# Performance work log

Hardware: AMD Instinct MI355X
Metric: run time of the kernel (lower is better)

The kernel has to match this reference:

```python
import jax, jax.numpy as jnp
import numpy as np

B, D_IN, D_H, D_OUT, D_INT = 1024, 2048, 4096, 2048, 1024


def fwht(x):
    """Fast Walsh-Hadamard transform over a length-2^k vector (unnormalized),
    faithful to the torch chunk/cat butterfly loop."""
    n = x.shape[0]
    k = int(n).bit_length() - 1
    for i in range(k):
        y = x.reshape(2 ** i, 2, -1)        # split butterfly level i
        x = jnp.stack([y[:, 0] + y[:, 1], y[:, 0] - y[:, 1]], axis=1)
    return x.reshape(n)


def fastfood(V, BB, Pi, GG, DD):
    """fastfood_torched: pad -> B*x -> H -> permute -> G* -> H -> slice/scale."""
    LL = BB.shape[0]
    vpad = jnp.zeros((LL,), V.dtype).at[: V.shape[0]].set(V)
    m5 = fwht(fwht(BB * vpad)[Pi] * GG)
    divisor = jnp.sqrt(LL * jnp.sum(GG * GG))
    return m5[:DD] / (divisor * np.sqrt(float(DD) / LL))


def _ff_vars(key, DD):
    LL = 1 << int(np.ceil(np.log2(DD)))
    k1, k2, k3 = jax.random.split(key, 3)
    BB = jnp.where(jax.random.uniform(k1, (LL,)) < 0.5, -1.0, 1.0).astype(jnp.float32)
    Pi = jax.random.permutation(k2, LL).astype(jnp.int32)
    GG = jax.random.normal(k3, (LL,), dtype=jnp.float32)
    return BB, Pi, GG


def setup_inputs():
    key = jax.random.key(0)
    ks = jax.random.split(key, 8)
    x = jax.random.normal(ks[0], (B, D_IN), dtype=jnp.float32)
    V = jax.random.normal(ks[1], (D_INT,), dtype=jnp.float32) * 0.01
    W1_0 = jax.random.normal(ks[2], (D_H, D_IN), dtype=jnp.float32) * 0.02
    b1_0 = jnp.zeros((D_H,), jnp.float32)
    W2_0 = jax.random.normal(ks[3], (D_OUT, D_H), dtype=jnp.float32) * 0.02
    b2_0 = jnp.zeros((D_OUT,), jnp.float32)
    BB_W1, Pi_W1, GG_W1 = _ff_vars(ks[4], D_H * D_IN)
    BB_b1, Pi_b1, GG_b1 = _ff_vars(ks[5], D_H)
    BB_W2, Pi_W2, GG_W2 = _ff_vars(ks[6], D_OUT * D_H)
    BB_b2, Pi_b2, GG_b2 = _ff_vars(ks[7], D_OUT)
    return dict(x=x, V=V, W1_0=W1_0, b1_0=b1_0, W2_0=W2_0, b2_0=b2_0,
                BB_W1=BB_W1, Pi_W1=Pi_W1, GG_W1=GG_W1,
                BB_b1=BB_b1, Pi_b1=Pi_b1, GG_b1=GG_b1,
                BB_W2=BB_W2, Pi_W2=Pi_W2, GG_W2=GG_W2,
                BB_b2=BB_b2, Pi_b2=Pi_b2, GG_b2=GG_b2)


def reference(x, V, W1_0, b1_0, W2_0, b2_0,
              BB_W1, Pi_W1, GG_W1, BB_b1, Pi_b1, GG_b1,
              BB_W2, Pi_W2, GG_W2, BB_b2, Pi_b2, GG_b2):
    # Reconstruct each parameter: theta = theta0 + fastfood(V).view(shape)
    W1 = W1_0 + fastfood(V, BB_W1, Pi_W1, GG_W1, D_H * D_IN).reshape(D_H, D_IN)
    b1 = b1_0 + fastfood(V, BB_b1, Pi_b1, GG_b1, D_H)
    W2 = W2_0 + fastfood(V, BB_W2, Pi_W2, GG_W2, D_OUT * D_H).reshape(D_OUT, D_H)
    b2 = b2_0 + fastfood(V, BB_b2, Pi_b2, GG_b2, D_OUT)
    # Wrapped module forward (2-layer MLP)
    h = jax.nn.relu(x @ W1.T + b1)
    return h @ W2.T + b2
```

## Files before the change

kernel.cpp:

```cpp
#include <hip/hip_runtime.h>
#include <hip/hip_bf16.h>
#include <stdint.h>


typedef __attribute__((ext_vector_type(8))) short bf16x8;
typedef __attribute__((ext_vector_type(4))) float f32x4;

__device__ __forceinline__ ushort f2bf(float f) {
  union { float f; uint32_t u; } v; v.f = f;
  return (ushort)((v.u + 0x7FFFu + ((v.u >> 16) & 1u)) >> 16);
}
__device__ __forceinline__ float bf2f(ushort u) {
  union { uint32_t u; float f; } v; v.u = (uint32_t)u << 16; return v.f;
}

__device__ __forceinline__ void gload_lds16(const void* g, void* l) {
  __builtin_amdgcn_global_load_lds(
      (const __attribute__((address_space(1))) void*)g,
      (__attribute__((address_space(3))) void*)l, 16, 0, 0);
}

template <int NN>
__device__ __forceinline__ void wht_inreg(float* v) {
#pragma unroll
  for (int h = 1; h < NN; h <<= 1)
#pragma unroll
    for (int g = 0; g < NN; g += (h << 1))
#pragma unroll
      for (int k = 0; k < h; ++k) {
        float a = v[g + k], b = v[g + k + h];
        v[g + k] = a + b; v[g + k + h] = a - b;
      }
}

__global__ __launch_bounds__(256) void make_t_kernel(
    const float* __restrict__ V, const float* __restrict__ BB1,
    const float* __restrict__ BB2, float* __restrict__ t1, float* __restrict__ t2) {
  __shared__ float ts[1024];
  const float* BB = blockIdx.x ? BB2 : BB1;
  float* t = blockIdx.x ? t2 : t1;
  int tid = threadIdx.x;
  for (int i = tid; i < 1024; i += 256) ts[i] = BB[i] * V[i];
  for (int st = 0; st < 10; ++st) {
    int half = 1 << st;
    __syncthreads();
    for (int j = tid; j < 512; j += 256) {
      int p = ((j >> st) << (st + 1)) | (j & (half - 1));
      float a = ts[p], b = ts[p + half];
      ts[p] = a + b; ts[p + half] = a - b;
    }
  }
  __syncthreads();
  for (int i = tid; i < 1024; i += 256) t[i] = ts[i];
}

__global__ __launch_bounds__(256) void make_bias_kernel(
    const float* __restrict__ V,
    const float* __restrict__ BB1, const int* __restrict__ Pi1, const float* __restrict__ GG1, const float* __restrict__ b10,
    const float* __restrict__ BB2, const int* __restrict__ Pi2, const float* __restrict__ GG2, const float* __restrict__ b20,
    float* __restrict__ ob1, float* __restrict__ ob2) {
  __shared__ float ts[1024];
  __shared__ float zs[4096];
  __shared__ float red[4];
  int tid = threadIdx.x;
  int which = blockIdx.x;
  int L = which ? 2048 : 4096;
  const float* BB = which ? BB2 : BB1;
  const int* Pi = which ? Pi2 : Pi1;
  const float* GG = which ? GG2 : GG1;
  const float* b0 = which ? b20 : b10;
  float* ob = which ? ob2 : ob1;

  for (int i = tid; i < 1024; i += 256) ts[i] = BB[i] * V[i];
  for (int st = 0; st < 10; ++st) {
    int half = 1 << st;
    __syncthreads();
    for (int j = tid; j < 512; j += 256) {
      int p = ((j >> st) << (st + 1)) | (j & (half - 1));
      float a = ts[p], b = ts[p + half];
      ts[p] = a + b; ts[p + half] = a - b;
    }
  }
  __syncthreads();
  float gsum = 0.f;
  for (int i = tid; i < L; i += 256) {
    int pi = Pi[i];
    float g = GG[i];
    gsum += g * g;
    zs[i] = ts[pi & 1023] * g;
  }
  for (int o = 32; o > 0; o >>= 1) gsum += __shfl_down(gsum, o);
  if ((tid & 63) == 0) red[tid >> 6] = gsum;
  __syncthreads();
  float ssum = red[0] + red[1] + red[2] + red[3];
  for (int st = 0; (1 << st) < L; ++st) {
    int half = 1 << st;
    __syncthreads();
    for (int j = tid; j < (L >> 1); j += 256) {
      int p = ((j >> st) << (st + 1)) | (j & (half - 1));
      float a = zs[p], b = zs[p + half];
      zs[p] = a + b; zs[p + half] = a - b;
    }
  }
  __syncthreads();
  float scale = rsqrtf((float)L * ssum);
  for (int i = tid; i < L; i += 256) ob[i] = b0[i] + zs[i] * scale;
}

__global__ __launch_bounds__(256) void ff_pass1(
    const int* __restrict__ Pi, const float* __restrict__ GG,
    const float* __restrict__ t, ushort* __restrict__ inter, float* __restrict__ partials) {
  __shared__ float ts[1024];
  __shared__ float zs[8448];
  __shared__ float red[4];
  int tid = threadIdx.x;
  size_t base = (size_t)blockIdx.x * 8192;
  for (int i = tid; i < 1024; i += 256) ts[i] = t[i];
  __syncthreads();
  float gsum = 0.f;
#pragma unroll 8
  for (int ii = 0; ii < 32; ++ii) {
    int i = ii * 256 + tid;
    int pi = Pi[base + i];
    float g = GG[base + i];
    gsum += g * g;
    zs[i + (i >> 5)] = ts[pi & 1023] * g;
  }
  for (int o = 32; o > 0; o >>= 1) gsum += __shfl_down(gsum, o);
  if ((tid & 63) == 0) red[tid >> 6] = gsum;
  __syncthreads();
  if (tid == 0) partials[blockIdx.x] = red[0] + red[1] + red[2] + red[3];

  float v[32];
  {
    int b0 = tid << 5;
#pragma unroll
    for (int r = 0; r < 32; ++r) { int i = b0 + r; v[r] = zs[i + (i >> 5)]; }
    wht_inreg<32>(v);
#pragma unroll
    for (int r = 0; r < 32; ++r) { int i = b0 + r; zs[i + (i >> 5)] = v[r]; }
  }
  __syncthreads();
  {
    int lo = tid & 31, hi = tid >> 5;
#pragma unroll
    for (int r = 0; r < 32; ++r) { int i = lo | (r << 5) | (hi << 10); v[r] = zs[i + (i >> 5)]; }
    wht_inreg<32>(v);
#pragma unroll
    for (int r = 0; r < 32; ++r) { int i = lo | (r << 5) | (hi << 10); zs[i + (i >> 5)] = v[r]; }
  }
  __syncthreads();
  {
    float w[32];
#pragma unroll
    for (int q = 0; q < 4; ++q)
#pragma unroll
      for (int r = 0; r < 8; ++r) { int i = tid + (q << 8) + (r << 10); w[q * 8 + r] = zs[i + (i >> 5)]; }
#pragma unroll
    for (int q = 0; q < 4; ++q) wht_inreg<8>(w + 8 * q);
#pragma unroll
    for (int q = 0; q < 4; ++q)
#pragma unroll
      for (int r = 0; r < 8; ++r)
        inter[base + tid + (q << 8) + (r << 10)] = f2bf(w[q * 8 + r]);
  }
}

__global__ __launch_bounds__(1024) void ff_pass2(
    const ushort* __restrict__ inter, const float* __restrict__ W0,
    const float* __restrict__ partials, ushort* __restrict__ Wb) {
  __shared__ float tile[1024 * 33];
  __shared__ float red2[16];
  int tid = threadIdx.x;
  int cb = blockIdx.x * 32;
  float s = partials[tid];
  for (int o = 32; o > 0; o >>= 1) s += __shfl_down(s, o);
  if ((tid & 63) == 0) red2[tid >> 6] = s;
#pragma unroll
  for (int it = 0; it < 8; ++it) {
    int u = it * 1024 + tid;
    int row = u >> 3, c4 = u & 7;
    ushort4 d = *(const ushort4*)(inter + (size_t)row * 8192 + cb + (c4 << 2));
    float* tp = &tile[row * 33 + (c4 << 2)];
    tp[0] = bf2f(d.x); tp[1] = bf2f(d.y); tp[2] = bf2f(d.z); tp[3] = bf2f(d.w);
  }
  __syncthreads();
  float ssum = 0.f;
#pragma unroll
  for (int k = 0; k < 16; ++k) ssum += red2[k];
  float sc = rsqrtf(8388608.f * ssum);

  float v[32];
  int c = tid & 31, g = tid >> 5;
#pragma unroll
  for (int r = 0; r < 32; ++r) v[r] = tile[(32 * g + r) * 33 + c];
  wht_inreg<32>(v);
#pragma unroll
  for (int r = 0; r < 32; ++r) tile[(32 * g + r) * 33 + c] = v[r];
  __syncthreads();
#pragma unroll
  for (int r = 0; r < 32; ++r) v[r] = tile[((r << 5) + g) * 33 + c];
  wht_inreg<32>(v);
#pragma unroll
  for (int r = 0; r < 32; ++r) {
    size_t gg = (size_t)((r << 5) + g) * 8192 + cb + c;
    Wb[gg] = f2bf(v[r] * sc + W0[gg]);
  }
}

__global__ __launch_bounds__(256) void cvt_f32_bf16(
    const float4* __restrict__ in, ushort4* __restrict__ out, int n4) {
  int i = blockIdx.x * 256 + threadIdx.x;
  if (i < n4) {
    float4 v = in[i];
    ushort4 o;
    o.x = f2bf(v.x); o.y = f2bf(v.y); o.z = f2bf(v.z); o.w = f2bf(v.w);
    out[i] = o;
  }
}

template <int EPI>
__global__ __launch_bounds__(256) void gemm_bt(
    const ushort* __restrict__ A, const ushort* __restrict__ B,
    const float* __restrict__ bias, ushort* __restrict__ Cb, float* __restrict__ Cf,
    int M, int N, int K, int nt) {
  __shared__ ushort As[2][128 * 64];
  __shared__ ushort Bs[2][128 * 64];
  const int tid = threadIdx.x;
  const int w = tid >> 6, l = tid & 63;
  const int wr = w >> 1, wc = w & 1;
  const int brow = blockIdx.y << 7, bcol = blockIdx.x << 7;
  const int lrow = l >> 3;
  const int csrc = ((l & 7) ^ lrow) << 3;
  const int l15 = l & 15;
  const int x7 = l15 & 7;
  const int kb = blockIdx.z * (nt << 6);
  f32x4 acc[4][4] = {};

  const ushort* pa = A + (size_t)(brow + (w << 5) + lrow) * K + kb + csrc;
  const ushort* pb = B + (size_t)(bcol + (w << 5) + lrow) * K + kb + csrc;
  const size_t K8 = (size_t)K << 3;

#define STAGE(buf, tt)                                                      \
  {                                                                         \
    const ushort* qa = pa + ((tt) << 6);                                    \
    const ushort* qb = pb + ((tt) << 6);                                    \
    _Pragma("unroll")                                                       \
    for (int i = 0; i < 4; ++i) {                                           \
      gload_lds16(qa + K8 * i, &As[buf][(((w << 2) + i) << 9)]);            \
      gload_lds16(qb + K8 * i, &Bs[buf][(((w << 2) + i) << 9)]);            \
    }                                                                       \
  }

  STAGE(0, 0);
  __syncthreads();
  for (int t = 0; t < nt; ++t) {
    int cur = t & 1;
    if (t + 1 < nt) STAGE(cur ^ 1, t + 1);
#pragma unroll
    for (int kk = 0; kk < 2; ++kk) {
      bf16x8 af[4], bfr[4];
      int c8 = (kk << 2) + (l >> 4);
#pragma unroll
      for (int m = 0; m < 4; ++m) {
        int ra = (wr << 6) + (m << 4) + l15;
        af[m] = *(const bf16x8*)&As[cur][(ra << 6) + ((c8 ^ x7) << 3)];
      }
#pragma unroll
      for (int n = 0; n < 4; ++n) {
        int rb = (wc << 6) + (n << 4) + l15;
        bfr[n] = *(const bf16x8*)&Bs[cur][(rb << 6) + ((c8 ^ x7) << 3)];
      }
#pragma unroll
      for (int m = 0; m < 4; ++m)
#pragma unroll
        for (int n = 0; n < 4; ++n)
          acc[m][n] = __builtin_amdgcn_mfma_f32_16x16x32_bf16(af[m], bfr[n], acc[m][n], 0, 0, 0);
    }
    __syncthreads();
  }
#undef STAGE

  if (EPI == 0) {
#pragma unroll
    for (int n = 0; n < 4; ++n) {
      int col = bcol + (wc << 6) + (n << 4) + l15;
      float bv = bias[col];
#pragma unroll
      for (int m = 0; m < 4; ++m) {
        int row0 = brow + (wr << 6) + (m << 4) + ((l >> 4) << 2);
#pragma unroll
        for (int j = 0; j < 4; ++j) {
          float vv = fmaxf(acc[m][n][j] + bv, 0.f);
          Cb[(size_t)(row0 + j) * N + col] = f2bf(vv);
        }
      }
    }
  } else {
    float* outp = Cf + (size_t)blockIdx.z * M * N;
#pragma unroll
    for (int n = 0; n < 4; ++n) {
      int col = bcol + (wc << 6) + (n << 4) + l15;
#pragma unroll
      for (int m = 0; m < 4; ++m) {
        int row0 = brow + (wr << 6) + (m << 4) + ((l >> 4) << 2);
#pragma unroll
        for (int j = 0; j < 4; ++j)
          outp[(size_t)(row0 + j) * N + col] = acc[m][n][j];
      }
    }
  }
}

__global__ __launch_bounds__(256) void reduce_out(
    const float4* __restrict__ P, const float* __restrict__ b2,
    float4* __restrict__ out) {
  int i = blockIdx.x * 256 + threadIdx.x;
  float4 a = P[i], b = P[i + 524288];
  const float4 bb = *(const float4*)(b2 + ((i & 511) << 2));
  float4 o;
  o.x = a.x + b.x + bb.x; o.y = a.y + b.y + bb.y;
  o.z = a.z + b.z + bb.z; o.w = a.w + b.w + bb.w;
  out[i] = o;
}

extern "C" void kernel_launch(void* const* d_in, const int* in_sizes, int n_in,
                              void* d_out, int out_size, void* d_ws, size_t ws_size,
                              hipStream_t stream) {
  const float* x     = (const float*)d_in[0];
  const float* V     = (const float*)d_in[1];
  const float* W1_0  = (const float*)d_in[2];
  const float* b1_0  = (const float*)d_in[3];
  const float* W2_0  = (const float*)d_in[4];
  const float* b2_0  = (const float*)d_in[5];
  const float* BB_W1 = (const float*)d_in[6];
  const int*   Pi_W1 = (const int*)d_in[7];
  const float* GG_W1 = (const float*)d_in[8];
  const float* BB_b1 = (const float*)d_in[9];
  const int*   Pi_b1 = (const int*)d_in[10];
  const float* GG_b1 = (const float*)d_in[11];
  const float* BB_W2 = (const float*)d_in[12];
  const int*   Pi_W2 = (const int*)d_in[13];
  const float* GG_W2 = (const float*)d_in[14];
  const float* BB_b2 = (const float*)d_in[15];
  const int*   Pi_b2 = (const int*)d_in[16];
  const float* GG_b2 = (const float*)d_in[17];
  float* out = (float*)d_out;

  const size_t MB = 1048576ull;
  char* ws = (char*)d_ws;
  ushort* inter = (ushort*)(ws);
  float*  P     = (float*)(ws);
  ushort* W1b   = (ushort*)(ws + 16 * MB);
  ushort* W2b   = (ushort*)(ws + 32 * MB);
  ushort* xb    = (ushort*)(ws + 48 * MB);
  ushort* hb    = (ushort*)(ws + 52 * MB);
  char*   S     = ws + 60 * MB;
  float*  t1    = (float*)(S);
  float*  t2    = (float*)(S + 4096);
  float*  b1    = (float*)(S + 8192);
  float*  b2    = (float*)(S + 8192 + 16384);
  float*  parts = (float*)(S + 8192 + 16384 + 8192);

  make_t_kernel<<<2, 256, 0, stream>>>(V, BB_W1, BB_W2, t1, t2);
  make_bias_kernel<<<2, 256, 0, stream>>>(V, BB_b1, Pi_b1, GG_b1, b1_0,
                                          BB_b2, Pi_b2, GG_b2, b2_0, b1, b2);
  cvt_f32_bf16<<<2048, 256, 0, stream>>>((const float4*)x, (ushort4*)xb, 524288);

  ff_pass1<<<1024, 256, 0, stream>>>(Pi_W1, GG_W1, t1, inter, parts);
  ff_pass2<<<256, 1024, 0, stream>>>(inter, W1_0, parts, W1b);
  ff_pass1<<<1024, 256, 0, stream>>>(Pi_W2, GG_W2, t2, inter, parts);
  ff_pass2<<<256, 1024, 0, stream>>>(inter, W2_0, parts, W2b);

  gemm_bt<0><<<dim3(32, 8, 1), 256, 0, stream>>>(xb, W1b, b1, hb, nullptr, 1024, 4096, 2048, 32);
  gemm_bt<1><<<dim3(16, 8, 2), 256, 0, stream>>>(hb, W2b, nullptr, nullptr, P, 1024, 2048, 4096, 32);
  reduce_out<<<2048, 256, 0, stream>>>((const float4*)P, b2, (float4*)out);
}
```

Before: 184.8 us.

## Batch fastfood passes for both weights, vectorize accesses, deepen GEMM pipeline

The W1 and W2 fastfood passes now run as single launches with twice the blocks, replacing two pairs of launches. Global loads and stores in both passes are widened to 16-byte vectors, and the WHT stage index mapping in pass1 is changed so the bf16 output can be stored contiguously. Pass2 now stages its result through LDS before writing coalesced short8 stores. The GEMM goes from a 2-stage to a 4-stage LDS ring with hand-placed vmcnt waits and raw barriers, which makes LDS use larger and depends on correct waitcnt accounting.

```diff
diff --git a/kernel.cpp b/kernel.cpp
--- a/kernel.cpp
+++ b/kernel.cpp
@@ -4,6 +4,7 @@
 
 
 typedef __attribute__((ext_vector_type(8))) short bf16x8;
+typedef __attribute__((ext_vector_type(8))) short short8;
 typedef __attribute__((ext_vector_type(4))) float f32x4;
 
 __device__ __forceinline__ ushort f2bf(float f) {
@@ -19,6 +20,12 @@
       (const __attribute__((address_space(1))) void*)g,
       (__attribute__((address_space(3))) void*)l, 16, 0, 0);
 }
+
+__device__ __forceinline__ void wait_vm16() { asm volatile("s_waitcnt vmcnt(16)" ::: "memory"); }
+__device__ __forceinline__ void wait_vm8()  { asm volatile("s_waitcnt vmcnt(8)"  ::: "memory"); }
+__device__ __forceinline__ void wait_vm0()  { asm volatile("s_waitcnt vmcnt(0)"  ::: "memory"); }
+__device__ __forceinline__ void wait_lgkm0(){ asm volatile("s_waitcnt lgkmcnt(0)" ::: "memory"); }
+__device__ __forceinline__ void barrier_raw(){ asm volatile("s_barrier" ::: "memory"); }
 
 template <int NN>
 __device__ __forceinline__ void wht_inreg(float* v) {
@@ -108,23 +115,42 @@
 }
 
 __global__ __launch_bounds__(256) void ff_pass1(
-    const int* __restrict__ Pi, const float* __restrict__ GG,
-    const float* __restrict__ t, ushort* __restrict__ inter, float* __restrict__ partials) {
+    const int* __restrict__ Pi1, const float* __restrict__ GG1,
+    const int* __restrict__ Pi2, const float* __restrict__ GG2,
+    const float* __restrict__ t1, const float* __restrict__ t2,
+    ushort* __restrict__ inter1, ushort* __restrict__ inter2,
+    float* __restrict__ partials) {
   __shared__ float ts[1024];
   __shared__ float zs[8448];
   __shared__ float red[4];
   int tid = threadIdx.x;
-  size_t base = (size_t)blockIdx.x * 8192;
+  int wsel = blockIdx.x >> 10;
+  int blk = blockIdx.x & 1023;
+  const int* Pi = wsel ? Pi2 : Pi1;
+  const float* GG = wsel ? GG2 : GG1;
+  const float* t = wsel ? t2 : t1;
+  ushort* inter = wsel ? inter2 : inter1;
+  size_t base = (size_t)blk * 8192;
+
   for (int i = tid; i < 1024; i += 256) ts[i] = t[i];
   __syncthreads();
+
+  const int4* Pi4 = (const int4*)(Pi + base);
+  const float4* GG4 = (const float4*)(GG + base);
   float gsum = 0.f;
-#pragma unroll 8
-  for (int ii = 0; ii < 32; ++ii) {
-    int i = ii * 256 + tid;
-    int pi = Pi[base + i];
-    float g = GG[base + i];
-    gsum += g * g;
-    zs[i + (i >> 5)] = ts[pi & 1023] * g;
+#pragma unroll
+  for (int q = 0; q < 8; ++q) {
+    int u = (q << 8) + tid;
+    int4 p4 = Pi4[u];
+    float4 g4 = GG4[u];
+    gsum += g4.x * g4.x + g4.y * g4.y + g4.z * g4.z + g4.w * g4.w;
+    int i0 = u << 2;
+    float4 z;
+    z.x = ts[p4.x & 1023] * g4.x;
+    z.y = ts[p4.y & 1023] * g4.y;
+    z.z = ts[p4.z & 1023] * g4.z;
+    z.w = ts[p4.w & 1023] * g4.w;
+    *(float4*)&zs[i0 + (i0 >> 5)] = z;
   }
   for (int o = 32; o > 0; o >>= 1) gsum += __shfl_down(gsum, o);
   if ((tid & 63) == 0) red[tid >> 6] = gsum;
@@ -133,56 +159,65 @@
 
   float v[32];
   {
-    int b0 = tid << 5;
-#pragma unroll
-    for (int r = 0; r < 32; ++r) { int i = b0 + r; v[r] = zs[i + (i >> 5)]; }
+    int o = (tid & 7) | ((tid >> 3) << 8);
+#pragma unroll
+    for (int r = 0; r < 32; ++r) { int i = o + (r << 3); v[r] = zs[i + (i >> 5)]; }
     wht_inreg<32>(v);
 #pragma unroll
-    for (int r = 0; r < 32; ++r) { int i = b0 + r; zs[i + (i >> 5)] = v[r]; }
+    for (int r = 0; r < 32; ++r) { int i = o + (r << 3); zs[i + (i >> 5)] = v[r]; }
   }
   __syncthreads();
   {
-    int lo = tid & 31, hi = tid >> 5;
-#pragma unroll
-    for (int r = 0; r < 32; ++r) { int i = lo | (r << 5) | (hi << 10); v[r] = zs[i + (i >> 5)]; }
+#pragma unroll
+    for (int r = 0; r < 32; ++r) { int i = tid | (r << 8); v[r] = zs[i + (i >> 5)]; }
     wht_inreg<32>(v);
 #pragma unroll
-    for (int r = 0; r < 32; ++r) { int i = lo | (r << 5) | (hi << 10); zs[i + (i >> 5)] = v[r]; }
+    for (int r = 0; r < 32; ++r) { int i = tid | (r << 8); zs[i + (i >> 5)] = v[r]; }
   }
   __syncthreads();
   {
-    float w[32];
-#pragma unroll
-    for (int q = 0; q < 4; ++q)
-#pragma unroll
-      for (int r = 0; r < 8; ++r) { int i = tid + (q << 8) + (r << 10); w[q * 8 + r] = zs[i + (i >> 5)]; }
-#pragma unroll
-    for (int q = 0; q < 4; ++q) wht_inreg<8>(w + 8 * q);
-#pragma unroll
-    for (int q = 0; q < 4; ++q)
-#pragma unroll
-      for (int r = 0; r < 8; ++r)
-        inter[base + tid + (q << 8) + (r << 10)] = f2bf(w[q * 8 + r]);
+    int tp = ((tid & 63) << 3) | ((tid >> 6) << 11);
+#pragma unroll
+    for (int j = 0; j < 4; ++j)
+#pragma unroll
+      for (int k = 0; k < 8; ++k) { int i = tp + (j << 9) + k; v[(j << 3) + k] = zs[i + (i >> 5)]; }
+#pragma unroll
+    for (int j = 0; j < 4; ++j) wht_inreg<8>(v + (j << 3));
+#pragma unroll
+    for (int j = 0; j < 4; ++j) {
+      short8 s;
+#pragma unroll
+      for (int k = 0; k < 8; ++k) s[k] = (short)f2bf(v[(j << 3) + k]);
+      *(short8*)(inter + base + tp + (j << 9)) = s;
+    }
   }
 }
 
 __global__ __launch_bounds__(1024) void ff_pass2(
-    const ushort* __restrict__ inter, const float* __restrict__ W0,
-    const float* __restrict__ partials, ushort* __restrict__ Wb) {
+    const ushort* __restrict__ inter1, const ushort* __restrict__ inter2,
+    const float* __restrict__ W01, const float* __restrict__ W02,
+    const float* __restrict__ partials,
+    ushort* __restrict__ W1b, ushort* __restrict__ W2b) {
   __shared__ float tile[1024 * 33];
   __shared__ float red2[16];
   int tid = threadIdx.x;
-  int cb = blockIdx.x * 32;
-  float s = partials[tid];
+  int wsel = blockIdx.x >> 8;
+  int cb = (blockIdx.x & 255) << 5;
+  const ushort* inter = wsel ? inter2 : inter1;
+  const float* W0 = wsel ? W02 : W01;
+  ushort* Wb = wsel ? W2b : W1b;
+
+  float s = partials[(wsel << 10) + tid];
   for (int o = 32; o > 0; o >>= 1) s += __shfl_down(s, o);
   if ((tid & 63) == 0) red2[tid >> 6] = s;
 #pragma unroll
-  for (int it = 0; it < 8; ++it) {
-    int u = it * 1024 + tid;
-    int row = u >> 3, c4 = u & 7;
-    ushort4 d = *(const ushort4*)(inter + (size_t)row * 8192 + cb + (c4 << 2));
-    float* tp = &tile[row * 33 + (c4 << 2)];
-    tp[0] = bf2f(d.x); tp[1] = bf2f(d.y); tp[2] = bf2f(d.z); tp[3] = bf2f(d.w);
+  for (int it = 0; it < 4; ++it) {
+    int u = (it << 10) + tid;
+    int row = u >> 2, c8 = (u & 3) << 3;
+    short8 d = *(const short8*)(inter + ((size_t)row << 13) + cb + c8);
+    float* tp = &tile[row * 33 + c8];
+#pragma unroll
+    for (int k = 0; k < 8; ++k) tp[k] = bf2f((ushort)d[k]);
   }
   __syncthreads();
   float ssum = 0.f;
@@ -193,18 +228,27 @@
   float v[32];
   int c = tid & 31, g = tid >> 5;
 #pragma unroll
-  for (int r = 0; r < 32; ++r) v[r] = tile[(32 * g + r) * 33 + c];
+  for (int r = 0; r < 32; ++r) v[r] = tile[((g << 5) + r) * 33 + c];
   wht_inreg<32>(v);
 #pragma unroll
-  for (int r = 0; r < 32; ++r) tile[(32 * g + r) * 33 + c] = v[r];
+  for (int r = 0; r < 32; ++r) tile[((g << 5) + r) * 33 + c] = v[r];
   __syncthreads();
 #pragma unroll
   for (int r = 0; r < 32; ++r) v[r] = tile[((r << 5) + g) * 33 + c];
   wht_inreg<32>(v);
 #pragma unroll
-  for (int r = 0; r < 32; ++r) {
-    size_t gg = (size_t)((r << 5) + g) * 8192 + cb + c;
-    Wb[gg] = f2bf(v[r] * sc + W0[gg]);
+  for (int r = 0; r < 32; ++r) tile[((r << 5) + g) * 33 + c] = v[r];
+  __syncthreads();
+#pragma unroll
+  for (int it = 0; it < 4; ++it) {
+    int u = (it << 10) + tid;
+    int row = u >> 2, c8 = (u & 3) << 3;
+    size_t gbase = ((size_t)row << 13) + cb + c8;
+    const float* tp = &tile[row * 33 + c8];
+    short8 o8;
+#pragma unroll
+    for (int k = 0; k < 8; ++k) o8[k] = (short)f2bf(tp[k] * sc + W0[gbase + k]);
+    *(short8*)(Wb + gbase) = o8;
   }
 }
 
@@ -219,13 +263,13 @@
   }
 }
 
-template <int EPI>
+template <int EPI, int NT>
 __global__ __launch_bounds__(256) void gemm_bt(
     const ushort* __restrict__ A, const ushort* __restrict__ B,
     const float* __restrict__ bias, ushort* __restrict__ Cb, float* __restrict__ Cf,
-    int M, int N, int K, int nt) {
-  __shared__ ushort As[2][128 * 64];
-  __shared__ ushort Bs[2][128 * 64];
+    int M, int N, int K) {
+  __shared__ ushort As[4][8192];
+  __shared__ ushort Bs[4][8192];
   const int tid = threadIdx.x;
   const int w = tid >> 6, l = tid & 63;
   const int wr = w >> 1, wc = w & 1;
@@ -234,7 +278,7 @@
   const int csrc = ((l & 7) ^ lrow) << 3;
   const int l15 = l & 15;
   const int x7 = l15 & 7;
-  const int kb = blockIdx.z * (nt << 6);
+  const int kb = blockIdx.z * (NT << 6);
   f32x4 acc[4][4] = {};
 
   const ushort* pa = A + (size_t)(brow + (w << 5) + lrow) * K + kb + csrc;
@@ -252,32 +296,34 @@
     }                                                                       \
   }
 
-  STAGE(0, 0);
-  __syncthreads();
-  for (int t = 0; t < nt; ++t) {
-    int cur = t & 1;
-    if (t + 1 < nt) STAGE(cur ^ 1, t + 1);
+  STAGE(0, 0); STAGE(1, 1); STAGE(2, 2);
+  for (int t = 0; t < NT; ++t) {
+    if (t < NT - 2) wait_vm16();
+    else if (t == NT - 2) wait_vm8();
+    else wait_vm0();
+    barrier_raw();
+    if (t + 3 < NT) STAGE((t + 3) & 3, t + 3);
+    const ushort* Acur = As[t & 3];
+    const ushort* Bcur = Bs[t & 3];
+    bf16x8 af[2][4], bfr[2][4];
 #pragma unroll
     for (int kk = 0; kk < 2; ++kk) {
-      bf16x8 af[4], bfr[4];
       int c8 = (kk << 2) + (l >> 4);
 #pragma unroll
-      for (int m = 0; m < 4; ++m) {
-        int ra = (wr << 6) + (m << 4) + l15;
-        af[m] = *(const bf16x8*)&As[cur][(ra << 6) + ((c8 ^ x7) << 3)];
-      }
-#pragma unroll
-      for (int n = 0; n < 4; ++n) {
-        int rb = (wc << 6) + (n << 4) + l15;
-        bfr[n] = *(const bf16x8*)&Bs[cur][(rb << 6) + ((c8 ^ x7) << 3)];
-      }
-#pragma unroll
       for (int m = 0; m < 4; ++m)
+        af[kk][m] = *(const bf16x8*)&Acur[(((wr << 6) + (m << 4) + l15) << 6) + ((c8 ^ x7) << 3)];
+#pragma unroll
+      for (int n = 0; n < 4; ++n)
+        bfr[kk][n] = *(const bf16x8*)&Bcur[(((wc << 6) + (n << 4) + l15) << 6) + ((c8 ^ x7) << 3)];
+    }
+    wait_lgkm0();
+#pragma unroll
+    for (int kk = 0; kk < 2; ++kk)
+#pragma unroll
+      for (int m = 0; m < 4; ++m)
 #pragma unroll
         for (int n = 0; n < 4; ++n)
-          acc[m][n] = __builtin_amdgcn_mfma_f32_16x16x32_bf16(af[m], bfr[n], acc[m][n], 0, 0, 0);
-    }
-    __syncthreads();
+          acc[m][n] = __builtin_amdgcn_mfma_f32_16x16x32_bf16(af[kk][m], bfr[kk][n], acc[m][n], 0, 0, 0);
   }
 #undef STAGE
 
@@ -349,30 +395,30 @@
 
   const size_t MB = 1048576ull;
   char* ws = (char*)d_ws;
-  ushort* inter = (ushort*)(ws);
-  float*  P     = (float*)(ws);
-  ushort* W1b   = (ushort*)(ws + 16 * MB);
-  ushort* W2b   = (ushort*)(ws + 32 * MB);
-  ushort* xb    = (ushort*)(ws + 48 * MB);
-  ushort* hb    = (ushort*)(ws + 52 * MB);
-  char*   S     = ws + 60 * MB;
-  float*  t1    = (float*)(S);
-  float*  t2    = (float*)(S + 4096);
-  float*  b1    = (float*)(S + 8192);
-  float*  b2    = (float*)(S + 8192 + 16384);
-  float*  parts = (float*)(S + 8192 + 16384 + 8192);
+  ushort* inter1 = (ushort*)(ws);
+  float*  P      = (float*)(ws);
+  ushort* inter2 = (ushort*)(ws + 16 * MB);
+  ushort* W1b    = (ushort*)(ws + 32 * MB);
+  ushort* W2b    = (ushort*)(ws + 48 * MB);
+  ushort* xb     = (ushort*)(ws + 64 * MB);
+  ushort* hb     = (ushort*)(ws + 68 * MB);
+  char*   S      = ws + 76 * MB;
+  float*  t1     = (float*)(S);
+  float*  t2     = (float*)(S + 4096);
+  float*  b1     = (float*)(S + 8192);
+  float*  b2     = (float*)(S + 8192 + 16384);
+  float*  parts  = (float*)(S + 8192 + 16384 + 8192);
 
   make_t_kernel<<<2, 256, 0, stream>>>(V, BB_W1, BB_W2, t1, t2);
   make_bias_kernel<<<2, 256, 0, stream>>>(V, BB_b1, Pi_b1, GG_b1, b1_0,
                                           BB_b2, Pi_b2, GG_b2, b2_0, b1, b2);
   cvt_f32_bf16<<<2048, 256, 0, stream>>>((const float4*)x, (ushort4*)xb, 524288);
 
-  ff_pass1<<<1024, 256, 0, stream>>>(Pi_W1, GG_W1, t1, inter, parts);
-  ff_pass2<<<256, 1024, 0, stream>>>(inter, W1_0, parts, W1b);
-  ff_pass1<<<1024, 256, 0, stream>>>(Pi_W2, GG_W2, t2, inter, parts);
-  ff_pass2<<<256, 1024, 0, stream>>>(inter, W2_0, parts, W2b);
-
-  gemm_bt<0><<<dim3(32, 8, 1), 256, 0, stream>>>(xb, W1b, b1, hb, nullptr, 1024, 4096, 2048, 32);
-  gemm_bt<1><<<dim3(16, 8, 2), 256, 0, stream>>>(hb, W2b, nullptr, nullptr, P, 1024, 2048, 4096, 32);
+  ff_pass1<<<2048, 256, 0, stream>>>(Pi_W1, GG_W1, Pi_W2, GG_W2, t1, t2,
+                                     inter1, inter2, parts);
+  ff_pass2<<<512, 1024, 0, stream>>>(inter1, inter2, W1_0, W2_0, parts, W1b, W2b);
+
+  gemm_bt<0, 32><<<dim3(32, 8, 1), 256, 0, stream>>>(xb, W1b, b1, hb, nullptr, 1024, 4096, 2048);
+  gemm_bt<1, 32><<<dim3(16, 8, 2), 256, 0, stream>>>(hb, W2b, nullptr, nullptr, P, 1024, 2048, 4096);
   reduce_out<<<2048, 256, 0, stream>>>((const float4*)P, b2, (float4*)out);
 }
```

After: 175.2 us. -5.2%, faster.
